# Optimization experiments

Hardware: AMD Instinct MI355X
Metric: run time of the kernel (lower is better)

Reference implementation:

```python
import jax, jax.numpy as jnp
import numpy as np

K = 7      # unfold_size
P = 3      # unfold_size // 2
EPS = 1e-5 # batchnorm eps


def _conv1x1(x, w, b=None):
    # x: (B,C,H,W), w: (O,C)
    y = jnp.einsum('bchw,oc->bohw', x, w)
    if b is not None:
        y = y + b[None, :, None, None]
    return y


def _bn(x, g, b, m, v):
    # eval-mode batchnorm over channel axis 1
    inv = jax.lax.rsqrt(v + EPS)
    return (x - m[None, :, None, None]) * (g * inv)[None, :, None, None] + b[None, :, None, None]


def setup_inputs() -> dict:
    key = jax.random.key(0)
    ks = jax.random.split(key, 18)
    B, C, MID, H, W = 8, 256, 64, 64, 64
    rn = lambda k, s, sc=1.0: jax.random.normal(k, s, dtype=jnp.float32) * sc
    ru = lambda k, s: jax.random.uniform(k, s, dtype=jnp.float32)
    return {
        'x':     rn(ks[0], (B, C, H, W)),
        'w_red': rn(ks[1], (MID, C), 0.05),
        'w_c':   rn(ks[2], (3, MID, MID, 3, 3), 0.05),
        'b_c':   rn(ks[3], (3, MID), 0.05),
        'bn_g':  ru(ks[4], (3, MID)) * 0.5 + 0.75,
        'bn_b':  rn(ks[5], (3, MID), 0.05),
        'bn_m':  rn(ks[6], (3, MID), 0.05),
        'bn_v':  ru(ks[7], (3, MID)) + 0.5,
        'w_out': rn(ks[8], (C, MID), 0.05),
        'b_out': rn(ks[9], (C,), 0.05),
        'bno_g': ru(ks[10], (C,)) * 0.5 + 0.75,
        'bno_b': rn(ks[11], (C,), 0.05),
        'bno_m': rn(ks[12], (C,), 0.05),
        'bno_v': ru(ks[13], (C,)) + 0.5,
        'w_f1':  rn(ks[14], (C, C), 0.05),
        'b_f1':  rn(ks[15], (C,), 0.05),
        'w_f2':  rn(ks[16], (C, C), 0.05),
        'b_f2':  rn(ks[17], (C,), 0.05),
    }


def reference(x, w_red, w_c, b_c, bn_g, bn_b, bn_m, bn_v,
              w_out, b_out, bno_g, bno_b, bno_m, bno_v,
              w_f1, b_f1, w_f2, b_f2):
    B, C, H, W = x.shape
    MID = w_red.shape[0]

    # channel reduction + L2 normalize over channels (F.normalize, eps=1e-12)
    q = _conv1x1(x, w_red)                                   # (B,MID,H,W)
    q = q / jnp.maximum(jnp.linalg.norm(q, axis=1, keepdims=True), 1e-12)

    # SelfCorrelationComputation: unfold KxK with padding P, multiply by center, clamp >= 0
    qp = jnp.pad(q, ((0, 0), (0, 0), (P, P), (P, P)))
    pats = jnp.stack([qp[:, :, i:i + H, j:j + W]
                      for i in range(K) for j in range(K)], axis=2)  # (B,MID,K*K,H,W)
    ss = jnp.maximum(pats * q[:, :, None], 0.0)              # (B,MID,49,H,W)

    # SelfSimilarityEncoder: conv3d with (1,ksize,ksize) kernel == batched 2D conv over (u,v)
    ss = ss.transpose(0, 3, 4, 1, 2).reshape(B * H * W, MID, K, K)  # (B*HW,MID,K,K)
    dn = ('NCHW', 'OIHW', 'NCHW')
    y = ss
    for i in range(3):  # unfold_size // 2 blocks; 7 -> 5 -> 3 -> 1
        y = jax.lax.conv_general_dilated(y, w_c[i], (1, 1), 'VALID', dimension_numbers=dn)
        y = y + b_c[i][None, :, None, None]
        y = jnp.maximum(_bn(y, bn_g[i], bn_b[i], bn_m[i], bn_v[i]), 0.0)
    y = y.mean(axis=(-1, -2)).reshape(B, H, W, MID).transpose(0, 3, 1, 2)  # (B,MID,H,W)
    feat = _bn(_conv1x1(y, w_out, b_out), bno_g, bno_b, bno_m, bno_v)      # (B,C,H,W)

    # residual + FFN (1x1 conv -> relu -> 1x1 conv)
    out = x + feat
    out = _conv1x1(jnp.maximum(_conv1x1(out, w_f1, b_f1), 0.0), w_f2, b_f2)
    return out
```

## Files before the change

kernel.cpp:

```cpp
#include <hip/hip_runtime.h>
#include <stdint.h>


typedef __attribute__((ext_vector_type(8))) __bf16 bf16x8;
typedef __attribute__((ext_vector_type(4))) float f32x4;

__device__ __forceinline__ ushort f2bf(float f) {
  uint32_t u = __builtin_bit_cast(uint32_t, f);
  u += 0x7fffu + ((u >> 16) & 1u);
  return (ushort)(u >> 16);
}
__device__ __forceinline__ float bfu(ushort h) {
  return __builtin_bit_cast(float, ((uint32_t)h) << 16);
}
__device__ __forceinline__ f32x4 mfma16(bf16x8 a, bf16x8 b, f32x4 c) {
  return __builtin_amdgcn_mfma_f32_16x16x32_bf16(a, b, c, 0, 0, 0);
}

union BV8 { uint4 v; ushort u[8]; };

#define OFF_WRT 0u
#define OFF_WCB 65536u
#define OFF_SHC 286720u
#define OFF_WOB 287488u
#define OFF_SHO 320256u
#define OFF_WF1 321280u
#define OFF_WF2 452352u
#define OFF_QN  583424u
#define OFF_Y   4777728u

__global__ __launch_bounds__(256) void k_prep(
    const float* __restrict__ w_red, const float* __restrict__ w_c, const float* __restrict__ b_c,
    const float* __restrict__ bn_g, const float* __restrict__ bn_b, const float* __restrict__ bn_m,
    const float* __restrict__ bn_v, const float* __restrict__ w_out, const float* __restrict__ b_out,
    const float* __restrict__ bno_g, const float* __restrict__ bno_b, const float* __restrict__ bno_m,
    const float* __restrict__ bno_v, const float* __restrict__ w_f1, const float* __restrict__ w_f2,
    float* __restrict__ w_red_t, ushort* __restrict__ wc_b, float* __restrict__ shift_c,
    ushort* __restrict__ w_out_b, float* __restrict__ shift_o,
    ushort* __restrict__ w_f1_b, ushort* __restrict__ w_f2_b)
{
  int i = blockIdx.x * 256 + threadIdx.x;
  if (i < 16384) {
    int c = i >> 6, m = i & 63;
    w_red_t[i] = w_red[m * 256 + c];
    return;
  }
  i -= 16384;
  if (i < 110592) {
    int c = i & 63, o = (i >> 6) & 63, st = i >> 12;
    int tap = st % 9, s = st / 9;
    float sc = bn_g[s * 64 + o] * rsqrtf(bn_v[s * 64 + o] + 1e-5f);
    wc_b[i] = f2bf(w_c[((s * 64 + o) * 64 + c) * 9 + tap] * sc);
    return;
  }
  i -= 110592;
  if (i < 192) {
    int s = i >> 6, o = i & 63;
    float sc = bn_g[s * 64 + o] * rsqrtf(bn_v[s * 64 + o] + 1e-5f);
    shift_c[i] = (b_c[i] - bn_m[i]) * sc + bn_b[i];
    return;
  }
  i -= 192;
  if (i < 16384) {
    int o = i >> 6;
    float sc = bno_g[o] * rsqrtf(bno_v[o] + 1e-5f);
    w_out_b[i] = f2bf(w_out[i] * sc);
    return;
  }
  i -= 16384;
  if (i < 256) {
    float sc = bno_g[i] * rsqrtf(bno_v[i] + 1e-5f);
    shift_o[i] = (b_out[i] - bno_m[i]) * sc + bno_b[i];
    return;
  }
  i -= 256;
  if (i < 65536) { w_f1_b[i] = f2bf(w_f1[i]); return; }
  i -= 65536;
  if (i < 65536) { w_f2_b[i] = f2bf(w_f2[i]); return; }
}

__global__ __launch_bounds__(256) void k_qnorm(
    const float* __restrict__ x, const float* __restrict__ w_red_t, ushort* __restrict__ qn)
{
  __shared__ float xs[64 * 64];
  __shared__ float wls[64 * 64];
  __shared__ float part[64 * 16];
  __shared__ float sinv[64];

  const int tid = threadIdx.x;
  const int pix0 = blockIdx.x * 64;
  const int b = pix0 >> 12;
  const int hw0 = pix0 & 4095;
  const int pxq = tid & 15, mq = tid >> 4;
  const int lr = tid >> 2, lseg = tid & 3;

  float acc[4][4] = {};

  for (int c0 = 0; c0 < 256; c0 += 64) {
    const float4* xg = (const float4*)(x + (size_t)(b * 256 + c0 + lr) * 4096 + hw0 + lseg * 16);
    float4* xd = (float4*)(xs + lr * 64 + lseg * 16);
    const float4* wg = (const float4*)(w_red_t + (c0 + lr) * 64 + lseg * 16);
    float4* wd = (float4*)(wls + lr * 64 + lseg * 16);
#pragma unroll
    for (int j = 0; j < 4; ++j) xd[j] = xg[j];
#pragma unroll
    for (int j = 0; j < 4; ++j) wd[j] = wg[j];
    __syncthreads();
    for (int c = 0; c < 64; ++c) {
      float4 xv = *(const float4*)(xs + c * 64 + pxq * 4);
      float4 wv = *(const float4*)(wls + c * 64 + mq * 4);
      float xa[4] = {xv.x, xv.y, xv.z, xv.w};
      float wa[4] = {wv.x, wv.y, wv.z, wv.w};
#pragma unroll
      for (int mi = 0; mi < 4; ++mi)
#pragma unroll
        for (int pi = 0; pi < 4; ++pi)
          acc[mi][pi] = fmaf(wa[mi], xa[pi], acc[mi][pi]);
    }
    __syncthreads();
  }

#pragma unroll
  for (int pi = 0; pi < 4; ++pi) {
    float s = 0.f;
#pragma unroll
    for (int mi = 0; mi < 4; ++mi) s += acc[mi][pi] * acc[mi][pi];
    part[(pxq * 4 + pi) * 16 + mq] = s;
  }
  __syncthreads();
  if (tid < 64) {
    float s = 0.f;
#pragma unroll
    for (int k = 0; k < 16; ++k) s += part[tid * 16 + k];
    sinv[tid] = 1.0f / fmaxf(sqrtf(s), 1e-12f);
  }
  __syncthreads();
#pragma unroll
  for (int pi = 0; pi < 4; ++pi) {
    const int px = pxq * 4 + pi;
    const float inv = sinv[px];
    ushort4 v;
    v.x = f2bf(acc[0][pi] * inv);
    v.y = f2bf(acc[1][pi] * inv);
    v.z = f2bf(acc[2][pi] * inv);
    v.w = f2bf(acc[3][pi] * inv);
    *(ushort4*)(qn + (size_t)(pix0 + px) * 64 + mq * 4) = v;
  }
}

#define SS_BYTES (49 * 16 * 64 * 2)
#define O1_BYTES (25 * 16 * 64 * 2)
#define SMEM_ENC (SS_BYTES + O1_BYTES)

__device__ __forceinline__ void load_af(bf16x8* af, const ushort* wbase, int o0, int n, int q) {
#pragma unroll
  for (int tap = 0; tap < 9; ++tap)
#pragma unroll
    for (int kc = 0; kc < 2; ++kc)
      af[tap * 2 + kc] = *(const bf16x8*)(wbase + (tap * 64 + o0 + n) * 64 + kc * 32 + q * 8);
}

__device__ __forceinline__ void store_act(ushort* buf, int pos, int n, int q, int o0,
                                          f32x4 acc, float4 sh) {
  ushort4 v;
  v.x = f2bf(fmaxf(acc[0] + sh.x, 0.0f));
  v.y = f2bf(fmaxf(acc[1] + sh.y, 0.0f));
  v.z = f2bf(fmaxf(acc[2] + sh.z, 0.0f));
  v.w = f2bf(fmaxf(acc[3] + sh.w, 0.0f));
  const int chunk = (o0 >> 3) + (q >> 1);
  *(ushort4*)(buf + (pos * 16 + n) * 64 + ((chunk ^ (n & 7)) * 8) + (q & 1) * 4) = v;
}

__global__ __launch_bounds__(512, 1) void k_encoder(
    const ushort* __restrict__ qn, const ushort* __restrict__ wc_b,
    const float* __restrict__ shift_c, ushort* __restrict__ yout)
{
  extern __shared__ char smem[];
  ushort* ss = (ushort*)smem;
  ushort* o1 = (ushort*)(smem + SS_BYTES);
  ushort* o2 = (ushort*)smem;

  const int tid = threadIdx.x;
  const int b = blockIdx.z;
  const int tr = blockIdx.y * 4;
  const int tc = blockIdx.x * 4;

  {
    const int p = tid & 15;
    const int g = tid >> 4;
    const int ph = tr + (p >> 2), pw = tc + (p & 3);
    const ushort* cen = qn + (size_t)((b << 12) + ph * 64 + pw) * 64;
    const int swp = p & 7;
#pragma unroll
    for (int ch = 0; ch < 8; ++ch) {
      BV8 cv; cv.v = *(const uint4*)(cen + ch * 8);
      float cf[8];
#pragma unroll
      for (int j = 0; j < 8; ++j) cf[j] = bfu(cv.u[j]);
      for (int uv = g; uv < 49; uv += 32) {
        const int du = uv / 7 - 3, dv = uv % 7 - 3;
        const int nh = ph + du, nw = pw + dv;
        BV8 ov;
        if ((unsigned)nh < 64u && (unsigned)nw < 64u) {
          BV8 nv; nv.v = *(const uint4*)(qn + (size_t)((b << 12) + nh * 64 + nw) * 64 + ch * 8);
#pragma unroll
          for (int j = 0; j < 8; ++j)
            ov.u[j] = f2bf(fmaxf(bfu(nv.u[j]) * cf[j], 0.0f));
        } else {
          ov.v = make_uint4(0u, 0u, 0u, 0u);
        }
        *(uint4*)(ss + (uv * 16 + p) * 64 + ((ch ^ swp) * 8)) = ov.v;
      }
    }
  }
  __syncthreads();

  const int lane = tid & 63, wv = tid >> 6;
  const int n = lane & 15, q = lane >> 4;
  const int o0 = (wv & 3) * 16;
  const int h = wv >> 2;
  const int sw = n & 7;
  const int rowoff = n * 64;
  const int c0 = ((0 + q) ^ sw) * 8;
  const int c1 = ((4 + q) ^ sw) * 8;

  bf16x8 af[18];
  const f32x4 zero = {0.f, 0.f, 0.f, 0.f};

  load_af(af, wc_b, o0, n, q);
  {
    const float4 sh = *(const float4*)(shift_c + o0 + q * 4);
    const int ubeg = h ? 3 : 0, uend = h ? 5 : 3;
    for (int u = ubeg; u < uend; ++u) {
      f32x4 acc[5][2];
#pragma unroll
      for (int v = 0; v < 5; ++v) { acc[v][0] = zero; acc[v][1] = zero; }
#pragma unroll
      for (int du = 0; du < 3; ++du) {
        const ushort* rowb = ss + (u + du) * 7 * 1024 + rowoff;
        bf16x8 rf0[7], rf1[7];
#pragma unroll
        for (int j = 0; j < 7; ++j) {
          rf0[j] = *(const bf16x8*)(rowb + j * 1024 + c0);
          rf1[j] = *(const bf16x8*)(rowb + j * 1024 + c1);
        }
#pragma unroll
        for (int dv = 0; dv < 3; ++dv) {
#pragma unroll
          for (int v = 0; v < 5; ++v) {
            acc[v][0] = mfma16(af[(du * 3 + dv) * 2],     rf0[v + dv], acc[v][0]);
            acc[v][1] = mfma16(af[(du * 3 + dv) * 2 + 1], rf1[v + dv], acc[v][1]);
          }
        }
      }
#pragma unroll
      for (int v = 0; v < 5; ++v)
        store_act(o1, u * 5 + v, n, q, o0, acc[v][0] + acc[v][1], sh);
    }
  }
  __syncthreads();

  load_af(af, wc_b + 9 * 4096, o0, n, q);
  {
    const float4 sh = *(const float4*)(shift_c + 64 + o0 + q * 4);
    const int ubeg = h ? 2 : 0, uend = h ? 3 : 2;
    for (int u = ubeg; u < uend; ++u) {
      f32x4 acc[3][2];
#pragma unroll
      for (int v = 0; v < 3; ++v) { acc[v][0] = zero; acc[v][1] = zero; }
#pragma unroll
      for (int du = 0; du < 3; ++du) {
        const ushort* rowb = o1 + (u + du) * 5 * 1024 + rowoff;
        bf16x8 rf0[5], rf1[5];
#pragma unroll
        for (int j = 0; j < 5; ++j) {
          rf0[j] = *(const bf16x8*)(rowb + j * 1024 + c0);
          rf1[j] = *(const bf16x8*)(rowb + j * 1024 + c1);
        }
#pragma unroll
        for (int dv = 0; dv < 3; ++dv) {
#pragma unroll
          for (int v = 0; v < 3; ++v) {
            acc[v][0] = mfma16(af[(du * 3 + dv) * 2],     rf0[v + dv], acc[v][0]);
            acc[v][1] = mfma16(af[(du * 3 + dv) * 2 + 1], rf1[v + dv], acc[v][1]);
          }
        }
      }
#pragma unroll
      for (int v = 0; v < 3; ++v)
        store_act(o2, u * 3 + v, n, q, o0, acc[v][0] + acc[v][1], sh);
    }
  }
  __syncthreads();

  if (h == 0) {
    load_af(af, wc_b + 18 * 4096, o0, n, q);
    const float4 sh = *(const float4*)(shift_c + 128 + o0 + q * 4);
    f32x4 a0 = zero, a1 = zero;
#pragma unroll
    for (int tap = 0; tap < 9; ++tap) {
      const ushort* rA = o2 + tap * 1024 + rowoff;
      a0 = mfma16(af[tap * 2],     *(const bf16x8*)(rA + c0), a0);
      a1 = mfma16(af[tap * 2 + 1], *(const bf16x8*)(rA + c1), a1);
    }
    f32x4 acc = a0 + a1;
    ushort4 v;
    v.x = f2bf(fmaxf(acc[0] + sh.x, 0.0f));
    v.y = f2bf(fmaxf(acc[1] + sh.y, 0.0f));
    v.z = f2bf(fmaxf(acc[2] + sh.z, 0.0f));
    v.w = f2bf(fmaxf(acc[3] + sh.w, 0.0f));
    const int ph = tr + (n >> 2), pw = tc + (n & 3);
    *(ushort4*)(yout + (size_t)((b << 12) + ph * 64 + pw) * 64 + o0 + q * 4) = v;
  }
}

#define SMEM_OUT (2 * 64 * 256 * 2)

__global__ __launch_bounds__(256) void k_out(
    const ushort* __restrict__ y, const float* __restrict__ x,
    const ushort* __restrict__ w_out_b, const float* __restrict__ shift_o,
    const ushort* __restrict__ w_f1_b, const float* __restrict__ b_f1,
    const ushort* __restrict__ w_f2_b, const float* __restrict__ b_f2,
    float* __restrict__ out)
{
  extern __shared__ char smem[];
  ushort* rls = (ushort*)smem;
  ushort* hls = (ushort*)(smem + 64 * 256 * 2);

  const int tid = threadIdx.x, lane = tid & 63, wv = tid >> 6;
  const int n = lane & 15, q = lane >> 4;
  const int pix0 = blockIdx.x * 64;
  const int b = pix0 >> 12, hw0 = pix0 & 4095;
  const int sw = n & 7;
  const f32x4 zero = {0.f, 0.f, 0.f, 0.f};

  {
    bf16x8 wa[8];
#pragma unroll
    for (int mt = 0; mt < 4; ++mt) {
      const int ob = wv * 64 + mt * 16;
      wa[mt * 2]     = *(const bf16x8*)(w_out_b + (ob + n) * 64 + q * 8);
      wa[mt * 2 + 1] = *(const bf16x8*)(w_out_b + (ob + n) * 64 + 32 + q * 8);
    }
    for (int nt = 0; nt < 4; ++nt) {
      const int px0 = nt * 16;
      const bf16x8 yb0 = *(const bf16x8*)(y + (size_t)(pix0 + px0 + n) * 64 + q * 8);
      const bf16x8 yb1 = *(const bf16x8*)(y + (size_t)(pix0 + px0 + n) * 64 + 32 + q * 8);
#pragma unroll
      for (int mt = 0; mt < 4; ++mt) {
        const int ob = wv * 64 + mt * 16;
        f32x4 acc = zero;
        acc = mfma16(wa[mt * 2], yb0, acc);
        acc = mfma16(wa[mt * 2 + 1], yb1, acc);
        const float4 sh = *(const float4*)(shift_o + ob + q * 4);
        const float sha[4] = {sh.x, sh.y, sh.z, sh.w};
        ushort tmp[4];
#pragma unroll
        for (int r = 0; r < 4; ++r) {
          const int o = ob + q * 4 + r;
          const float xv = x[(size_t)(b * 256 + o) * 4096 + hw0 + px0 + n];
          tmp[r] = f2bf(xv + acc[r] + sha[r]);
        }
        ushort4 v; v.x = tmp[0]; v.y = tmp[1]; v.z = tmp[2]; v.w = tmp[3];
        const int chunk = (ob >> 3) + (q >> 1);
        *(ushort4*)(rls + (px0 + n) * 256 + ((chunk ^ sw) * 8) + (q & 1) * 4) = v;
      }
    }
  }
  __syncthreads();

  {
    bf16x8 wf[32];
#pragma unroll
    for (int mt = 0; mt < 4; ++mt)
#pragma unroll
      for (int kc = 0; kc < 8; ++kc)
        wf[mt * 8 + kc] = *(const bf16x8*)(w_f1_b + (size_t)(wv * 64 + mt * 16 + n) * 256 + kc * 32 + q * 8);
    for (int nt = 0; nt < 4; ++nt) {
      const int px0 = nt * 16;
      bf16x8 rb[8];
#pragma unroll
      for (int kc = 0; kc < 8; ++kc)
        rb[kc] = *(const bf16x8*)(rls + (px0 + n) * 256 + (((kc * 4 + q) ^ sw) * 8));
#pragma unroll
      for (int mt = 0; mt < 4; ++mt) {
        const int ob = wv * 64 + mt * 16;
        f32x4 a0 = zero, a1 = zero;
#pragma unroll
        for (int kc = 0; kc < 8; kc += 2) {
          a0 = mfma16(wf[mt * 8 + kc], rb[kc], a0);
          a1 = mfma16(wf[mt * 8 + kc + 1], rb[kc + 1], a1);
        }
        f32x4 acc = a0 + a1;
        const float4 bb = *(const float4*)(b_f1 + ob + q * 4);
        const float bba[4] = {bb.x, bb.y, bb.z, bb.w};
        ushort tmp[4];
#pragma unroll
        for (int r = 0; r < 4; ++r) tmp[r] = f2bf(fmaxf(acc[r] + bba[r], 0.0f));
        ushort4 v; v.x = tmp[0]; v.y = tmp[1]; v.z = tmp[2]; v.w = tmp[3];
        const int chunk = (ob >> 3) + (q >> 1);
        *(ushort4*)(hls + (px0 + n) * 256 + ((chunk ^ sw) * 8) + (q & 1) * 4) = v;
      }
    }
  }
  __syncthreads();

  {
    bf16x8 wf[32];
#pragma unroll
    for (int mt = 0; mt < 4; ++mt)
#pragma unroll
      for (int kc = 0; kc < 8; ++kc)
        wf[mt * 8 + kc] = *(const bf16x8*)(w_f2_b + (size_t)(wv * 64 + mt * 16 + n) * 256 + kc * 32 + q * 8);
    for (int nt = 0; nt < 4; ++nt) {
      const int px0 = nt * 16;
      bf16x8 rb[8];
#pragma unroll
      for (int kc = 0; kc < 8; ++kc)
        rb[kc] = *(const bf16x8*)(hls + (px0 + n) * 256 + (((kc * 4 + q) ^ sw) * 8));
#pragma unroll
      for (int mt = 0; mt < 4; ++mt) {
        const int ob = wv * 64 + mt * 16;
        f32x4 a0 = zero, a1 = zero;
#pragma unroll
        for (int kc = 0; kc < 8; kc += 2) {
          a0 = mfma16(wf[mt * 8 + kc], rb[kc], a0);
          a1 = mfma16(wf[mt * 8 + kc + 1], rb[kc + 1], a1);
        }
        f32x4 acc = a0 + a1;
        const float4 bb = *(const float4*)(b_f2 + ob + q * 4);
        const float bba[4] = {bb.x, bb.y, bb.z, bb.w};
#pragma unroll
        for (int r = 0; r < 4; ++r) {
          const int o = ob + q * 4 + r;
          out[(size_t)(b * 256 + o) * 4096 + hw0 + px0 + n] = acc[r] + bba[r];
        }
      }
    }
  }
}

extern "C" void kernel_launch(void* const* d_in, const int* in_sizes, int n_in,
                              void* d_out, int out_size, void* d_ws, size_t ws_size,
                              hipStream_t stream) {
  const float* x     = (const float*)d_in[0];
  const float* w_red = (const float*)d_in[1];
  const float* w_c   = (const float*)d_in[2];
  const float* b_c   = (const float*)d_in[3];
  const float* bn_g  = (const float*)d_in[4];
  const float* bn_b  = (const float*)d_in[5];
  const float* bn_m  = (const float*)d_in[6];
  const float* bn_v  = (const float*)d_in[7];
  const float* w_out = (const float*)d_in[8];
  const float* b_out = (const float*)d_in[9];
  const float* bno_g = (const float*)d_in[10];
  const float* bno_b = (const float*)d_in[11];
  const float* bno_m = (const float*)d_in[12];
  const float* bno_v = (const float*)d_in[13];
  const float* w_f1  = (const float*)d_in[14];
  const float* b_f1  = (const float*)d_in[15];
  const float* w_f2  = (const float*)d_in[16];
  const float* b_f2  = (const float*)d_in[17];

  char* ws = (char*)d_ws;
  float*  w_red_t = (float*)(ws + OFF_WRT);
  ushort* wc_b    = (ushort*)(ws + OFF_WCB);
  float*  shift_c = (float*)(ws + OFF_SHC);
  ushort* w_out_b = (ushort*)(ws + OFF_WOB);
  float*  shift_o = (float*)(ws + OFF_SHO);
  ushort* w_f1_b  = (ushort*)(ws + OFF_WF1);
  ushort* w_f2_b  = (ushort*)(ws + OFF_WF2);
  ushort* qnb     = (ushort*)(ws + OFF_QN);
  ushort* yb      = (ushort*)(ws + OFF_Y);

  k_prep<<<1074, 256, 0, stream>>>(w_red, w_c, b_c, bn_g, bn_b, bn_m, bn_v,
                                   w_out, b_out, bno_g, bno_b, bno_m, bno_v,
                                   w_f1, w_f2,
                                   w_red_t, wc_b, shift_c, w_out_b, shift_o, w_f1_b, w_f2_b);
  k_qnorm<<<512, 256, 0, stream>>>(x, w_red_t, qnb);
  k_encoder<<<dim3(16, 16, 8), 512, SMEM_ENC, stream>>>(qnb, wc_b, shift_c, yb);
  k_out<<<512, 256, SMEM_OUT, stream>>>(yb, x, w_out_b, shift_o, w_f1_b, b_f1, w_f2_b, b_f2,
                                        (float*)d_out);
}
```

Before: 323.8 us.

## Use MFMA for qnorm, double encoder threads, use packed bf16 conversion

Several changes land at once. The channel reduction in k_qnorm moves from fp32 FMA to bf16 MFMA, with the input transposed into LDS and the norm reduced through lane shuffles. The encoder runs 1024 threads per block, and the conv output rows are split across 16 waves with templated per-row MFMA loops, so weights are read per tap instead of kept in registers. Hardware packed bf16 conversion replaces manual rounding in every store. The aim is more parallelism and less ALU work, at the cost of extra weight reloads from memory, bf16 precision in the reduction GEMM, and register pressure under the new launch bounds.

```diff
diff --git a/kernel.cpp b/kernel.cpp
--- a/kernel.cpp
+++ b/kernel.cpp
@@ -13,13 +13,23 @@
 __device__ __forceinline__ float bfu(ushort h) {
   return __builtin_bit_cast(float, ((uint32_t)h) << 16);
 }
+__device__ __forceinline__ unsigned int pk2(float lo, float hi) {
+#if __has_builtin(__builtin_amdgcn_cvt_pk_bf16_f32)
+  auto r = __builtin_amdgcn_cvt_pk_bf16_f32(lo, hi);
+  unsigned int u;
+  __builtin_memcpy(&u, &r, 4);
+  return u;
+#else
+  return (unsigned int)f2bf(lo) | ((unsigned int)f2bf(hi) << 16);
+#endif
+}
 __device__ __forceinline__ f32x4 mfma16(bf16x8 a, bf16x8 b, f32x4 c) {
   return __builtin_amdgcn_mfma_f32_16x16x32_bf16(a, b, c, 0, 0, 0);
 }
 
 union BV8 { uint4 v; ushort u[8]; };
 
-#define OFF_WRT 0u
+#define OFF_WRB 0u
 #define OFF_WCB 65536u
 #define OFF_SHC 286720u
 #define OFF_WOB 287488u
@@ -35,14 +45,13 @@
     const float* __restrict__ bn_v, const float* __restrict__ w_out, const float* __restrict__ b_out,
     const float* __restrict__ bno_g, const float* __restrict__ bno_b, const float* __restrict__ bno_m,
     const float* __restrict__ bno_v, const float* __restrict__ w_f1, const float* __restrict__ w_f2,
-    float* __restrict__ w_red_t, ushort* __restrict__ wc_b, float* __restrict__ shift_c,
+    ushort* __restrict__ w_red_b, ushort* __restrict__ wc_b, float* __restrict__ shift_c,
     ushort* __restrict__ w_out_b, float* __restrict__ shift_o,
     ushort* __restrict__ w_f1_b, ushort* __restrict__ w_f2_b)
 {
   int i = blockIdx.x * 256 + threadIdx.x;
   if (i < 16384) {
-    int c = i >> 6, m = i & 63;
-    w_red_t[i] = w_red[m * 256 + c];
+    w_red_b[i] = f2bf(w_red[i]);
     return;
   }
   i -= 16384;
@@ -79,72 +88,72 @@
   if (i < 65536) { w_f2_b[i] = f2bf(w_f2[i]); return; }
 }
 
+#define QN_STRIDE 264
+
 __global__ __launch_bounds__(256) void k_qnorm(
-    const float* __restrict__ x, const float* __restrict__ w_red_t, ushort* __restrict__ qn)
+    const float* __restrict__ x, const ushort* __restrict__ w_red_b, ushort* __restrict__ qn)
 {
-  __shared__ float xs[64 * 64];
-  __shared__ float wls[64 * 64];
-  __shared__ float part[64 * 16];
-  __shared__ float sinv[64];
+  __shared__ ushort xt[64 * QN_STRIDE];
 
   const int tid = threadIdx.x;
   const int pix0 = blockIdx.x * 64;
-  const int b = pix0 >> 12;
-  const int hw0 = pix0 & 4095;
-  const int pxq = tid & 15, mq = tid >> 4;
-  const int lr = tid >> 2, lseg = tid & 3;
-
-  float acc[4][4] = {};
-
-  for (int c0 = 0; c0 < 256; c0 += 64) {
-    const float4* xg = (const float4*)(x + (size_t)(b * 256 + c0 + lr) * 4096 + hw0 + lseg * 16);
-    float4* xd = (float4*)(xs + lr * 64 + lseg * 16);
-    const float4* wg = (const float4*)(w_red_t + (c0 + lr) * 64 + lseg * 16);
-    float4* wd = (float4*)(wls + lr * 64 + lseg * 16);
-#pragma unroll
-    for (int j = 0; j < 4; ++j) xd[j] = xg[j];
-#pragma unroll
-    for (int j = 0; j < 4; ++j) wd[j] = wg[j];
-    __syncthreads();
-    for (int c = 0; c < 64; ++c) {
-      float4 xv = *(const float4*)(xs + c * 64 + pxq * 4);
-      float4 wv = *(const float4*)(wls + c * 64 + mq * 4);
-      float xa[4] = {xv.x, xv.y, xv.z, xv.w};
-      float wa[4] = {wv.x, wv.y, wv.z, wv.w};
-#pragma unroll
-      for (int mi = 0; mi < 4; ++mi)
-#pragma unroll
-        for (int pi = 0; pi < 4; ++pi)
-          acc[mi][pi] = fmaf(wa[mi], xa[pi], acc[mi][pi]);
-    }
-    __syncthreads();
-  }
-
-#pragma unroll
-  for (int pi = 0; pi < 4; ++pi) {
-    float s = 0.f;
-#pragma unroll
-    for (int mi = 0; mi < 4; ++mi) s += acc[mi][pi] * acc[mi][pi];
-    part[(pxq * 4 + pi) * 16 + mq] = s;
-  }
-  __syncthreads();
-  if (tid < 64) {
-    float s = 0.f;
-#pragma unroll
-    for (int k = 0; k < 16; ++k) s += part[tid * 16 + k];
-    sinv[tid] = 1.0f / fmaxf(sqrtf(s), 1e-12f);
-  }
-  __syncthreads();
-#pragma unroll
-  for (int pi = 0; pi < 4; ++pi) {
-    const int px = pxq * 4 + pi;
-    const float inv = sinv[px];
-    ushort4 v;
-    v.x = f2bf(acc[0][pi] * inv);
-    v.y = f2bf(acc[1][pi] * inv);
-    v.z = f2bf(acc[2][pi] * inv);
-    v.w = f2bf(acc[3][pi] * inv);
-    *(ushort4*)(qn + (size_t)(pix0 + px) * 64 + mq * 4) = v;
+  const int b = pix0 >> 12, hw0 = pix0 & 4095;
+
+  {
+    const int cl = tid >> 2, hq = tid & 3;
+    for (int cb = 0; cb < 4; ++cb) {
+      const int c = cb * 64 + cl;
+      const float* src = x + (size_t)(b * 256 + c) * 4096 + hw0 + hq * 16;
+#pragma unroll
+      for (int j = 0; j < 4; ++j) {
+        float4 v = *(const float4*)(src + j * 4);
+        const int hw = hq * 16 + j * 4;
+        xt[(hw + 0) * QN_STRIDE + c] = f2bf(v.x);
+        xt[(hw + 1) * QN_STRIDE + c] = f2bf(v.y);
+        xt[(hw + 2) * QN_STRIDE + c] = f2bf(v.z);
+        xt[(hw + 3) * QN_STRIDE + c] = f2bf(v.w);
+      }
+    }
+  }
+  __syncthreads();
+
+  const int lane = tid & 63, w = tid >> 6;
+  const int n = lane & 15, q = lane >> 4;
+  const int px = w * 16 + n;
+  const f32x4 zero = {0.f, 0.f, 0.f, 0.f};
+
+  bf16x8 bfr[8];
+#pragma unroll
+  for (int kc = 0; kc < 8; ++kc)
+    bfr[kc] = *(const bf16x8*)(xt + px * QN_STRIDE + kc * 32 + q * 8);
+
+  f32x4 acc[4];
+#pragma unroll
+  for (int mt = 0; mt < 4; ++mt) {
+    f32x4 a0 = zero, a1 = zero;
+#pragma unroll
+    for (int kc = 0; kc < 8; kc += 2) {
+      a0 = mfma16(*(const bf16x8*)(w_red_b + (mt * 16 + n) * 256 + kc * 32 + q * 8), bfr[kc], a0);
+      a1 = mfma16(*(const bf16x8*)(w_red_b + (mt * 16 + n) * 256 + (kc + 1) * 32 + q * 8), bfr[kc + 1], a1);
+    }
+    acc[mt] = a0 + a1;
+  }
+
+  float s = 0.f;
+#pragma unroll
+  for (int mt = 0; mt < 4; ++mt)
+#pragma unroll
+    for (int r = 0; r < 4; ++r) s += acc[mt][r] * acc[mt][r];
+  s += __shfl_xor(s, 16, 64);
+  s += __shfl_xor(s, 32, 64);
+  const float inv = 1.0f / fmaxf(sqrtf(s), 1e-12f);
+
+#pragma unroll
+  for (int mt = 0; mt < 4; ++mt) {
+    uint2 wv;
+    wv.x = pk2(acc[mt][0] * inv, acc[mt][1] * inv);
+    wv.y = pk2(acc[mt][2] * inv, acc[mt][3] * inv);
+    *(uint2*)(qn + (size_t)(pix0 + px) * 64 + mt * 16 + q * 4) = wv;
   }
 }
 
@@ -152,26 +161,53 @@
 #define O1_BYTES (25 * 16 * 64 * 2)
 #define SMEM_ENC (SS_BYTES + O1_BYTES)
 
-__device__ __forceinline__ void load_af(bf16x8* af, const ushort* wbase, int o0, int n, int q) {
-#pragma unroll
-  for (int tap = 0; tap < 9; ++tap)
-#pragma unroll
-    for (int kc = 0; kc < 2; ++kc)
-      af[tap * 2 + kc] = *(const bf16x8*)(wbase + (tap * 64 + o0 + n) * 64 + kc * 32 + q * 8);
-}
-
 __device__ __forceinline__ void store_act(ushort* buf, int pos, int n, int q, int o0,
                                           f32x4 acc, float4 sh) {
-  ushort4 v;
-  v.x = f2bf(fmaxf(acc[0] + sh.x, 0.0f));
-  v.y = f2bf(fmaxf(acc[1] + sh.y, 0.0f));
-  v.z = f2bf(fmaxf(acc[2] + sh.z, 0.0f));
-  v.w = f2bf(fmaxf(acc[3] + sh.w, 0.0f));
+  uint2 wv;
+  wv.x = pk2(fmaxf(acc[0] + sh.x, 0.0f), fmaxf(acc[1] + sh.y, 0.0f));
+  wv.y = pk2(fmaxf(acc[2] + sh.z, 0.0f), fmaxf(acc[3] + sh.w, 0.0f));
   const int chunk = (o0 >> 3) + (q >> 1);
-  *(ushort4*)(buf + (pos * 16 + n) * 64 + ((chunk ^ (n & 7)) * 8) + (q & 1) * 4) = v;
-}
-
-__global__ __launch_bounds__(512, 1) void k_encoder(
+  *(uint2*)(buf + (pos * 16 + n) * 64 + ((chunk ^ (n & 7)) * 8) + (q & 1) * 4) = wv;
+}
+
+template<int NV, int IW, int OW>
+__device__ __forceinline__ void conv_row(
+    const ushort* __restrict__ inb, ushort* __restrict__ outb,
+    const ushort* __restrict__ wst, const float4 sh,
+    int u, int vlo, int o0, int n, int q, int rowoff, int c0, int c1)
+{
+  const f32x4 zero = {0.f, 0.f, 0.f, 0.f};
+  f32x4 acc[NV];
+#pragma unroll
+  for (int v = 0; v < NV; ++v) acc[v] = zero;
+#pragma unroll
+  for (int du = 0; du < 3; ++du) {
+    const ushort* rowb = inb + ((u + du) * IW + vlo) * 1024 + rowoff;
+#pragma unroll
+    for (int kc = 0; kc < 2; ++kc) {
+      const int cc = kc ? c1 : c0;
+      const int wofs = kc * 32 + q * 8;
+      bf16x8 a[3];
+#pragma unroll
+      for (int dv = 0; dv < 3; ++dv)
+        a[dv] = *(const bf16x8*)(wst + ((du * 3 + dv) * 64 + o0 + n) * 64 + wofs);
+      bf16x8 rf[NV + 2];
+#pragma unroll
+      for (int j = 0; j < NV + 2; ++j)
+        rf[j] = *(const bf16x8*)(rowb + j * 1024 + cc);
+#pragma unroll
+      for (int dv = 0; dv < 3; ++dv)
+#pragma unroll
+        for (int v = 0; v < NV; ++v)
+          acc[v] = mfma16(a[dv], rf[v + dv], acc[v]);
+    }
+  }
+#pragma unroll
+  for (int v = 0; v < NV; ++v)
+    store_act(outb, u * OW + vlo + v, n, q, o0, acc[v], sh);
+}
+
+__global__ __launch_bounds__(1024, 4) void k_encoder(
     const ushort* __restrict__ qn, const ushort* __restrict__ wc_b,
     const float* __restrict__ shift_c, ushort* __restrict__ yout)
 {
@@ -188,129 +224,99 @@
   {
     const int p = tid & 15;
     const int g = tid >> 4;
-    const int ph = tr + (p >> 2), pw = tc + (p & 3);
-    const ushort* cen = qn + (size_t)((b << 12) + ph * 64 + pw) * 64;
-    const int swp = p & 7;
-#pragma unroll
-    for (int ch = 0; ch < 8; ++ch) {
-      BV8 cv; cv.v = *(const uint4*)(cen + ch * 8);
-      float cf[8];
-#pragma unroll
-      for (int j = 0; j < 8; ++j) cf[j] = bfu(cv.u[j]);
-      for (int uv = g; uv < 49; uv += 32) {
-        const int du = uv / 7 - 3, dv = uv % 7 - 3;
-        const int nh = ph + du, nw = pw + dv;
-        BV8 ov;
-        if ((unsigned)nh < 64u && (unsigned)nw < 64u) {
-          BV8 nv; nv.v = *(const uint4*)(qn + (size_t)((b << 12) + nh * 64 + nw) * 64 + ch * 8);
+    if (g < 49) {
+      const int ph = tr + (p >> 2), pw = tc + (p & 3);
+      const ushort* cen = qn + (size_t)((b << 12) + ph * 64 + pw) * 64;
+      const int swp = p & 7;
+      const int du = g / 7 - 3, dv = g % 7 - 3;
+      const int nh = ph + du, nw = pw + dv;
+      const bool ok = ((unsigned)nh < 64u) && ((unsigned)nw < 64u);
+      const ushort* nb = qn + (size_t)((b << 12) + nh * 64 + nw) * 64;
+      ushort* dst = ss + (g * 16 + p) * 64;
+#pragma unroll
+      for (int ch = 0; ch < 8; ++ch) {
+        uint4 ov;
+        if (ok) {
+          BV8 cv; cv.v = *(const uint4*)(cen + ch * 8);
+          BV8 nv; nv.v = *(const uint4*)(nb + ch * 8);
+          float pr[8];
 #pragma unroll
           for (int j = 0; j < 8; ++j)
-            ov.u[j] = f2bf(fmaxf(bfu(nv.u[j]) * cf[j], 0.0f));
+            pr[j] = fmaxf(bfu(nv.u[j]) * bfu(cv.u[j]), 0.0f);
+          ov.x = pk2(pr[0], pr[1]); ov.y = pk2(pr[2], pr[3]);
+          ov.z = pk2(pr[4], pr[5]); ov.w = pk2(pr[6], pr[7]);
         } else {
-          ov.v = make_uint4(0u, 0u, 0u, 0u);
+          ov = make_uint4(0u, 0u, 0u, 0u);
         }
-        *(uint4*)(ss + (uv * 16 + p) * 64 + ((ch ^ swp) * 8)) = ov.v;
+        *(uint4*)(dst + ((ch ^ swp) * 8)) = ov;
       }
     }
   }
   __syncthreads();
 
-  const int lane = tid & 63, wv = tid >> 6;
+  const int lane = tid & 63, wvi = tid >> 6;
   const int n = lane & 15, q = lane >> 4;
-  const int o0 = (wv & 3) * 16;
-  const int h = wv >> 2;
+  const int ot = wvi & 3, grp = wvi >> 2;
+  const int o0 = ot * 16;
   const int sw = n & 7;
   const int rowoff = n * 64;
   const int c0 = ((0 + q) ^ sw) * 8;
   const int c1 = ((4 + q) ^ sw) * 8;
-
-  bf16x8 af[18];
   const f32x4 zero = {0.f, 0.f, 0.f, 0.f};
 
-  load_af(af, wc_b, o0, n, q);
   {
     const float4 sh = *(const float4*)(shift_c + o0 + q * 4);
-    const int ubeg = h ? 3 : 0, uend = h ? 5 : 3;
-    for (int u = ubeg; u < uend; ++u) {
-      f32x4 acc[5][2];
-#pragma unroll
-      for (int v = 0; v < 5; ++v) { acc[v][0] = zero; acc[v][1] = zero; }
-#pragma unroll
-      for (int du = 0; du < 3; ++du) {
-        const ushort* rowb = ss + (u + du) * 7 * 1024 + rowoff;
-        bf16x8 rf0[7], rf1[7];
-#pragma unroll
-        for (int j = 0; j < 7; ++j) {
-          rf0[j] = *(const bf16x8*)(rowb + j * 1024 + c0);
-          rf1[j] = *(const bf16x8*)(rowb + j * 1024 + c1);
-        }
-#pragma unroll
-        for (int dv = 0; dv < 3; ++dv) {
-#pragma unroll
-          for (int v = 0; v < 5; ++v) {
-            acc[v][0] = mfma16(af[(du * 3 + dv) * 2],     rf0[v + dv], acc[v][0]);
-            acc[v][1] = mfma16(af[(du * 3 + dv) * 2 + 1], rf1[v + dv], acc[v][1]);
-          }
-        }
-      }
-#pragma unroll
-      for (int v = 0; v < 5; ++v)
-        store_act(o1, u * 5 + v, n, q, o0, acc[v][0] + acc[v][1], sh);
-    }
-  }
-  __syncthreads();
-
-  load_af(af, wc_b + 9 * 4096, o0, n, q);
+    const ushort* w1 = wc_b;
+    if (grp == 0) {
+      conv_row<5, 7, 5>(ss, o1, w1, sh, 0, 0, o0, n, q, rowoff, c0, c1);
+      conv_row<2, 7, 5>(ss, o1, w1, sh, 1, 0, o0, n, q, rowoff, c0, c1);
+    } else if (grp == 1) {
+      conv_row<3, 7, 5>(ss, o1, w1, sh, 1, 2, o0, n, q, rowoff, c0, c1);
+      conv_row<3, 7, 5>(ss, o1, w1, sh, 2, 0, o0, n, q, rowoff, c0, c1);
+    } else if (grp == 2) {
+      conv_row<2, 7, 5>(ss, o1, w1, sh, 2, 3, o0, n, q, rowoff, c0, c1);
+      conv_row<4, 7, 5>(ss, o1, w1, sh, 3, 0, o0, n, q, rowoff, c0, c1);
+    } else {
+      conv_row<1, 7, 5>(ss, o1, w1, sh, 3, 4, o0, n, q, rowoff, c0, c1);
+      conv_row<5, 7, 5>(ss, o1, w1, sh, 4, 0, o0, n, q, rowoff, c0, c1);
+    }
+  }
+  __syncthreads();
+
   {
     const float4 sh = *(const float4*)(shift_c + 64 + o0 + q * 4);
-    const int ubeg = h ? 2 : 0, uend = h ? 3 : 2;
-    for (int u = ubeg; u < uend; ++u) {
-      f32x4 acc[3][2];
-#pragma unroll
-      for (int v = 0; v < 3; ++v) { acc[v][0] = zero; acc[v][1] = zero; }
-#pragma unroll
-      for (int du = 0; du < 3; ++du) {
-        const ushort* rowb = o1 + (u + du) * 5 * 1024 + rowoff;
-        bf16x8 rf0[5], rf1[5];
-#pragma unroll
-        for (int j = 0; j < 5; ++j) {
-          rf0[j] = *(const bf16x8*)(rowb + j * 1024 + c0);
-          rf1[j] = *(const bf16x8*)(rowb + j * 1024 + c1);
-        }
-#pragma unroll
-        for (int dv = 0; dv < 3; ++dv) {
-#pragma unroll
-          for (int v = 0; v < 3; ++v) {
-            acc[v][0] = mfma16(af[(du * 3 + dv) * 2],     rf0[v + dv], acc[v][0]);
-            acc[v][1] = mfma16(af[(du * 3 + dv) * 2 + 1], rf1[v + dv], acc[v][1]);
-          }
-        }
-      }
-#pragma unroll
-      for (int v = 0; v < 3; ++v)
-        store_act(o2, u * 3 + v, n, q, o0, acc[v][0] + acc[v][1], sh);
-    }
-  }
-  __syncthreads();
-
-  if (h == 0) {
-    load_af(af, wc_b + 18 * 4096, o0, n, q);
+    const ushort* w2 = wc_b + 9 * 4096;
+    if (grp == 0) {
+      conv_row<3, 5, 3>(o1, o2, w2, sh, 0, 0, o0, n, q, rowoff, c0, c1);
+    } else if (grp == 1) {
+      conv_row<2, 5, 3>(o1, o2, w2, sh, 1, 0, o0, n, q, rowoff, c0, c1);
+    } else if (grp == 2) {
+      conv_row<1, 5, 3>(o1, o2, w2, sh, 1, 2, o0, n, q, rowoff, c0, c1);
+      conv_row<1, 5, 3>(o1, o2, w2, sh, 2, 0, o0, n, q, rowoff, c0, c1);
+    } else {
+      conv_row<2, 5, 3>(o1, o2, w2, sh, 2, 1, o0, n, q, rowoff, c0, c1);
+    }
+  }
+  __syncthreads();
+
+  if (grp == 0) {
     const float4 sh = *(const float4*)(shift_c + 128 + o0 + q * 4);
+    const ushort* w3 = wc_b + 18 * 4096;
     f32x4 a0 = zero, a1 = zero;
 #pragma unroll
     for (int tap = 0; tap < 9; ++tap) {
       const ushort* rA = o2 + tap * 1024 + rowoff;
-      a0 = mfma16(af[tap * 2],     *(const bf16x8*)(rA + c0), a0);
-      a1 = mfma16(af[tap * 2 + 1], *(const bf16x8*)(rA + c1), a1);
+      a0 = mfma16(*(const bf16x8*)(w3 + (tap * 64 + o0 + n) * 64 + q * 8),
+                  *(const bf16x8*)(rA + c0), a0);
+      a1 = mfma16(*(const bf16x8*)(w3 + (tap * 64 + o0 + n) * 64 + 32 + q * 8),
+                  *(const bf16x8*)(rA + c1), a1);
     }
     f32x4 acc = a0 + a1;
-    ushort4 v;
-    v.x = f2bf(fmaxf(acc[0] + sh.x, 0.0f));
-    v.y = f2bf(fmaxf(acc[1] + sh.y, 0.0f));
-    v.z = f2bf(fmaxf(acc[2] + sh.z, 0.0f));
-    v.w = f2bf(fmaxf(acc[3] + sh.w, 0.0f));
+    uint2 wv2;
+    wv2.x = pk2(fmaxf(acc[0] + sh.x, 0.0f), fmaxf(acc[1] + sh.y, 0.0f));
+    wv2.y = pk2(fmaxf(acc[2] + sh.z, 0.0f), fmaxf(acc[3] + sh.w, 0.0f));
     const int ph = tr + (n >> 2), pw = tc + (n & 3);
-    *(ushort4*)(yout + (size_t)((b << 12) + ph * 64 + pw) * 64 + o0 + q * 4) = v;
+    *(uint2*)(yout + (size_t)((b << 12) + ph * 64 + pw) * 64 + o0 + q * 4) = wv2;
   }
 }
 
@@ -354,16 +360,16 @@
         acc = mfma16(wa[mt * 2 + 1], yb1, acc);
         const float4 sh = *(const float4*)(shift_o + ob + q * 4);
         const float sha[4] = {sh.x, sh.y, sh.z, sh.w};
-        ushort tmp[4];
+        float t[4];
 #pragma unroll
         for (int r = 0; r < 4; ++r) {
           const int o = ob + q * 4 + r;
           const float xv = x[(size_t)(b * 256 + o) * 4096 + hw0 + px0 + n];
-          tmp[r] = f2bf(xv + acc[r] + sha[r]);
+          t[r] = xv + acc[r] + sha[r];
         }
-        ushort4 v; v.x = tmp[0]; v.y = tmp[1]; v.z = tmp[2]; v.w = tmp[3];
+        uint2 v; v.x = pk2(t[0], t[1]); v.y = pk2(t[2], t[3]);
         const int chunk = (ob >> 3) + (q >> 1);
-        *(ushort4*)(rls + (px0 + n) * 256 + ((chunk ^ sw) * 8) + (q & 1) * 4) = v;
+        *(uint2*)(rls + (px0 + n) * 256 + ((chunk ^ sw) * 8) + (q & 1) * 4) = v;
       }
     }
   }
@@ -393,13 +399,11 @@
         }
         f32x4 acc = a0 + a1;
         const float4 bb = *(const float4*)(b_f1 + ob + q * 4);
-        const float bba[4] = {bb.x, bb.y, bb.z, bb.w};
-        ushort tmp[4];
-#pragma unroll
-        for (int r = 0; r < 4; ++r) tmp[r] = f2bf(fmaxf(acc[r] + bba[r], 0.0f));
-        ushort4 v; v.x = tmp[0]; v.y = tmp[1]; v.z = tmp[2]; v.w = tmp[3];
+        uint2 v;
+        v.x = pk2(fmaxf(acc[0] + bb.x, 0.0f), fmaxf(acc[1] + bb.y, 0.0f));
+        v.y = pk2(fmaxf(acc[2] + bb.z, 0.0f), fmaxf(acc[3] + bb.w, 0.0f));
         const int chunk = (ob >> 3) + (q >> 1);
-        *(ushort4*)(hls + (px0 + n) * 256 + ((chunk ^ sw) * 8) + (q & 1) * 4) = v;
+        *(uint2*)(hls + (px0 + n) * 256 + ((chunk ^ sw) * 8) + (q & 1) * 4) = v;
       }
     }
   }
@@ -463,7 +467,7 @@
   const float* b_f2  = (const float*)d_in[17];
 
   char* ws = (char*)d_ws;
-  float*  w_red_t = (float*)(ws + OFF_WRT);
+  ushort* w_red_b = (ushort*)(ws + OFF_WRB);
   ushort* wc_b    = (ushort*)(ws + OFF_WCB);
   float*  shift_c = (float*)(ws + OFF_SHC);
   ushort* w_out_b = (ushort*)(ws + OFF_WOB);
@@ -476,9 +480,9 @@
   k_prep<<<1074, 256, 0, stream>>>(w_red, w_c, b_c, bn_g, bn_b, bn_m, bn_v,
                                    w_out, b_out, bno_g, bno_b, bno_m, bno_v,
                                    w_f1, w_f2,
-                                   w_red_t, wc_b, shift_c, w_out_b, shift_o, w_f1_b, w_f2_b);
-  k_qnorm<<<512, 256, 0, stream>>>(x, w_red_t, qnb);
-  k_encoder<<<dim3(16, 16, 8), 512, SMEM_ENC, stream>>>(qnb, wc_b, shift_c, yb);
+                                   w_red_b, wc_b, shift_c, w_out_b, shift_o, w_f1_b, w_f2_b);
+  k_qnorm<<<512, 256, 0, stream>>>(x, w_red_b, qnb);
+  k_encoder<<<dim3(16, 16, 8), 1024, SMEM_ENC, stream>>>(qnb, wc_b, shift_c, yb);
   k_out<<<512, 256, SMEM_OUT, stream>>>(yb, x, w_out_b, shift_o, w_f1_b, b_f1, w_f2_b, b_f2,
                                         (float*)d_out);
 }
```

Measured after the change: 362.0 us. +11.8%, slower.
